# Kernel optimization log

Measured on AMD Instinct MI355X. Metric: run time of the kernel, lower is better.

Reference implementation:

```python
import jax, jax.numpy as jnp
import numpy as np

HIDDEN = 2048
NUM_HEADS = 16
HEAD_DIM = HIDDEN // NUM_HEADS  # 128
B, S = 2, 2048


def setup_inputs() -> dict:
    key = jax.random.key(0)
    ks = jax.random.split(key, 16)
    w = lambda k, shp: (jax.random.normal(k, shp, jnp.float32) * 0.02)
    return {
        "query": jax.random.normal(ks[0], (B, S, HIDDEN), jnp.float32),
        "key": jax.random.normal(ks[1], (B, S, HIDDEN), jnp.float32),
        "value": jax.random.normal(ks[2], (B, S, HIDDEN), jnp.float32),
        "Wq": w(ks[3], (HIDDEN, HIDDEN)), "bq": jnp.zeros((HIDDEN,), jnp.float32),
        "Wk": w(ks[4], (HIDDEN, HIDDEN)), "bk": jnp.zeros((HIDDEN,), jnp.float32),
        "Wv": w(ks[5], (HIDDEN, HIDDEN)), "bv": jnp.zeros((HIDDEN,), jnp.float32),
        "Wo": w(ks[6], (HIDDEN, HIDDEN)), "bo": jnp.zeros((HIDDEN,), jnp.float32),
        "Wf1": w(ks[7], (HEAD_DIM, 2 * HEAD_DIM)), "bf1": jnp.zeros((2 * HEAD_DIM,), jnp.float32),
        "Wf2": w(ks[8], (2 * HEAD_DIM, HEAD_DIM)), "bf2": jnp.zeros((HEAD_DIM,), jnp.float32),
    }


def reference(query, key, value, Wq, bq, Wk, bk, Wv, bv, Wo, bo, Wf1, bf1, Wf2, bf2):
    b, s, _ = query.shape

    def split_heads(x):  # [b,s,H] -> [b,h,s,d]
        return x.reshape(b, s, NUM_HEADS, HEAD_DIM).transpose(0, 2, 1, 3)

    def feature_map(x):  # MLP on last dim: d -> 2d -> relu -> d
        return jax.nn.relu(x @ Wf1 + bf1) @ Wf2 + bf2

    Q = feature_map(split_heads(query @ Wq + bq))
    K = feature_map(split_heads(key @ Wk + bk))
    V = split_heads(value @ Wv + bv)

    # K^T V per head: [b,h,d,e]
    KV = jnp.einsum("bhsd,bhse->bhde", K, V)
    QKV = jnp.einsum("bhsd,bhde->bhse", Q, KV)
    # denominator: sum of all K entries per (b,h) -> scalar per head
    denom = jnp.sum(K, axis=(-2, -1), keepdims=True) + 1e-8
    QKV = QKV / denom

    context = QKV.transpose(0, 2, 1, 3).reshape(b, s, HIDDEN)
    output = context @ Wo + bo

    attn_weights = jnp.full((b, NUM_HEADS, s, s), 1.0 / s, dtype=query.dtype)
    return output, attn_weights
```

## Files before the change

### kernel.cpp

```cpp
#include <hip/hip_runtime.h>


typedef __bf16 bf16_t;
typedef __bf16 bf16x8 __attribute__((ext_vector_type(8)));
typedef __bf16 bf16x4 __attribute__((ext_vector_type(4)));
typedef float  f32x4  __attribute__((ext_vector_type(4)));

#define FILLV (1.0f / 2048.0f)

#define VMCNT2() asm volatile("s_waitcnt vmcnt(2)" ::: "memory")
#define VMCNT0() asm volatile("s_waitcnt vmcnt(0)" ::: "memory")
#define LGKM0()  asm volatile("s_waitcnt lgkmcnt(0)" ::: "memory")
#define BAR()    __builtin_amdgcn_s_barrier()
#define SCHED0() __builtin_amdgcn_sched_barrier(0)

__device__ __forceinline__ void gload16(const void* g, void* l) {
  __builtin_amdgcn_global_load_lds(
      (__attribute__((address_space(1))) void*)(g),
      (__attribute__((address_space(3))) void*)(l), 16, 0, 0);
}

__device__ __forceinline__ void stage_half(const bf16_t* __restrict__ g,
                                           int h, unsigned char* ldsT, int t) {
  const bf16_t* gh = g + (long)h * 128 * 2048;
  unsigned char* lh = ldsT + h * 16384;
#pragma unroll
  for (int i = 0; i < 2; ++i) {
    const int c = t + i * 512;
    const int r = c >> 3;
    const int cc = ((c & 7) ^ (r & 7)) * 8;
    gload16(gh + (long)r * 2048 + cc, lh + c * 16);
  }
}

__device__ __forceinline__ bf16x8 lds_frag(const unsigned char* base,
                                           int row, int kelem) {
  int byte = row * 128 + kelem * 2;
  byte ^= (row & 7) << 4;
  return *(const bf16x8*)(base + byte);
}

__global__ __launch_bounds__(512, 2) void proj_gemm8(
    const bf16_t* __restrict__ A, const bf16_t* __restrict__ Wt,
    const float* __restrict__ bq, const float* __restrict__ bk,
    const float* __restrict__ bv, bf16_t* __restrict__ C,
    float* __restrict__ attn)
{
  __shared__ __align__(16) unsigned char smem[131072];
  const int t = threadIdx.x;
  const int lane = t & 63;
  const int wid = t >> 6;
  const int wr = wid >> 2, wc = wid & 3;
  const int bid = blockIdx.x;
  const int bx = bid & 7, by = bid >> 3;
  const int which = by >> 4;
  const bf16_t* Ab = A + (long)by * 256 * 2048;
  const bf16_t* Bb = Wt + (long)which * 4194304 + (long)bx * 256 * 2048;
  const float* bias = which == 0 ? bq : (which == 1 ? bk : bv);

  const int lr = lane & 15;
  const int l8 = (lane >> 4) * 8;
  const f32x4 fv = {FILLV, FILLV, FILLV, FILLV};

  f32x4 acc[8][4];
#pragma unroll
  for (int i = 0; i < 8; ++i)
#pragma unroll
    for (int j = 0; j < 4; ++j) acc[i][j] = (f32x4){0.f, 0.f, 0.f, 0.f};

  stage_half(Ab, 0, smem, t);
  stage_half(Ab, 1, smem, t);
  stage_half(Bb, 0, smem + 32768, t);
  stage_half(Bb, 1, smem + 32768, t);

  bf16x8 aF[4][2], bF[4][2];

  for (int kt = 0; kt < 32; ++kt) {
    const int cur = kt & 1;
    unsigned char* curA = smem + cur * 65536;
    unsigned char* curB = curA + 32768;
    unsigned char* nxtA = smem + (cur ^ 1) * 65536;
    unsigned char* nxtB = nxtA + 32768;
    const bool hn = kt < 31;
    const bf16_t* An = Ab + (kt + 1) * 64;
    const bf16_t* Bn = Bb + (kt + 1) * 64;
    const int arow = wr * 128 + lr;
    const int brow = wc * 64 + lr;
    f32x4* fillp = (f32x4*)attn + ((long)kt * 384 + bid) * 3 * 512 + t;

    if (hn) { stage_half(An, 0, nxtA, t); VMCNT2(); }
    else    { VMCNT0(); }
    BAR();
#pragma unroll
    for (int mi = 0; mi < 4; ++mi)
#pragma unroll
      for (int kk = 0; kk < 2; ++kk)
        aF[mi][kk] = lds_frag(curA, arow + mi * 16, kk * 32 + l8);
#pragma unroll
    for (int ni = 0; ni < 2; ++ni)
#pragma unroll
      for (int kk = 0; kk < 2; ++kk)
        bF[ni][kk] = lds_frag(curB, brow + ni * 16, kk * 32 + l8);
    LGKM0(); SCHED0();
    __builtin_amdgcn_s_setprio(1);
#pragma unroll
    for (int mi = 0; mi < 4; ++mi)
#pragma unroll
      for (int ni = 0; ni < 2; ++ni)
#pragma unroll
        for (int kk = 0; kk < 2; ++kk)
          acc[mi][ni] = __builtin_amdgcn_mfma_f32_16x16x32_bf16(
              aF[mi][kk], bF[ni][kk], acc[mi][ni], 0, 0, 0);
    __builtin_amdgcn_s_setprio(0);
    BAR();

    if (hn) stage_half(An, 1, nxtA, t);
    __builtin_nontemporal_store(fv, fillp);
#pragma unroll
    for (int ni = 0; ni < 2; ++ni)
#pragma unroll
      for (int kk = 0; kk < 2; ++kk)
        bF[2 + ni][kk] = lds_frag(curB, brow + (2 + ni) * 16, kk * 32 + l8);
    BAR(); LGKM0(); SCHED0();
    __builtin_amdgcn_s_setprio(1);
#pragma unroll
    for (int mi = 0; mi < 4; ++mi)
#pragma unroll
      for (int ni = 0; ni < 2; ++ni)
#pragma unroll
        for (int kk = 0; kk < 2; ++kk)
          acc[mi][2 + ni] = __builtin_amdgcn_mfma_f32_16x16x32_bf16(
              aF[mi][kk], bF[2 + ni][kk], acc[mi][2 + ni], 0, 0, 0);
    __builtin_amdgcn_s_setprio(0);
    BAR();

    if (hn) stage_half(Bn, 0, nxtB, t);
    __builtin_nontemporal_store(fv, fillp + 512);
#pragma unroll
    for (int mi = 0; mi < 4; ++mi)
#pragma unroll
      for (int kk = 0; kk < 2; ++kk)
        aF[mi][kk] = lds_frag(curA, arow + 64 + mi * 16, kk * 32 + l8);
    BAR(); LGKM0(); SCHED0();
    __builtin_amdgcn_s_setprio(1);
#pragma unroll
    for (int mi = 0; mi < 4; ++mi)
#pragma unroll
      for (int ni = 0; ni < 2; ++ni)
#pragma unroll
        for (int kk = 0; kk < 2; ++kk)
          acc[4 + mi][ni] = __builtin_amdgcn_mfma_f32_16x16x32_bf16(
              aF[mi][kk], bF[ni][kk], acc[4 + mi][ni], 0, 0, 0);
    __builtin_amdgcn_s_setprio(0);
    BAR();

    if (hn) stage_half(Bn, 1, nxtB, t);
    __builtin_nontemporal_store(fv, fillp + 1024);
    BAR(); LGKM0(); SCHED0();
    __builtin_amdgcn_s_setprio(1);
#pragma unroll
    for (int mi = 0; mi < 4; ++mi)
#pragma unroll
      for (int ni = 0; ni < 2; ++ni)
#pragma unroll
        for (int kk = 0; kk < 2; ++kk)
          acc[4 + mi][2 + ni] = __builtin_amdgcn_mfma_f32_16x16x32_bf16(
              aF[mi][kk], bF[2 + ni][kk], acc[4 + mi][2 + ni], 0, 0, 0);
    __builtin_amdgcn_s_setprio(0);
    BAR();
  }

  const int row0 = by * 256 + wr * 128;
  const int col0 = bx * 256 + wc * 64;
#pragma unroll
  for (int mi = 0; mi < 8; ++mi) {
#pragma unroll
    for (int ni = 0; ni < 4; ++ni) {
      const int col = col0 + ni * 16 + lr;
      const float bvv = bias[col];
#pragma unroll
      for (int j = 0; j < 4; ++j) {
        const int row = row0 + mi * 16 + (lane >> 4) * 4 + j;
        C[(long)row * 2048 + col] = (bf16_t)(acc[mi][ni][j] + bvv);
      }
    }
  }
}

template<bool RELU, bool OUTF32, bool BIAS, int FILLMODE>
__global__ __launch_bounds__(256) void gemm_bt(
    const bf16_t* __restrict__ A, const bf16_t* __restrict__ Bt,
    const float* __restrict__ bias, void* __restrict__ C,
    int K, int lda, int ldb, int ldc,
    long aBatchB, long aBatchH, long bBatchB, long bBatchH,
    long cBatchB, long cBatchH, int HperB,
    float* __restrict__ attn, long fillBase, long fillBase2, int fillSlots)
{
  __shared__ bf16_t As[128 * 64];
  __shared__ bf16_t Bs[128 * 64];

  const int z  = blockIdx.z;
  const int zb = z / HperB, zh = z % HperB;
  const bf16_t* Ab = A  + (long)zb * aBatchB + (long)zh * aBatchH
                        + (long)blockIdx.y * 128 * lda;
  const bf16_t* Bb = Bt + (long)zb * bBatchB + (long)zh * bBatchH
                        + (long)blockIdx.x * 128 * ldb;

  const int t = threadIdx.x;
  const int lane = t & 63, w = t >> 6;
  const int wm = (w >> 1) * 64, wn = (w & 1) * 64;
  const int p = ((int)blockIdx.z * gridDim.y + blockIdx.y) * gridDim.x
                + blockIdx.x;

  f32x4 acc[4][4];
#pragma unroll
  for (int i = 0; i < 4; ++i)
#pragma unroll
    for (int j = 0; j < 4; ++j) acc[i][j] = (f32x4){0.f, 0.f, 0.f, 0.f};

  for (int k0 = 0; k0 < K; k0 += 64) {
#pragma unroll
    for (int i = 0; i < 4; ++i) {
      int c = i * 256 + t;
      int row = c >> 3, col = (c & 7) * 8;
      gload16(Ab + (long)row * lda + k0 + col, &As[c * 8]);
      gload16(Bb + (long)row * ldb + k0 + col, &Bs[c * 8]);
    }
    if constexpr (FILLMODE == 3) {
      const f32x4 fv = {FILLV, FILLV, FILLV, FILLV};
      const long nB = (long)gridDim.x * gridDim.y * gridDim.z;
      long s0 = fillBase + (((long)(k0 >> 6) * nB + p) * 3) * 256 + t;
      __builtin_nontemporal_store(fv, (f32x4*)attn + s0);
      __builtin_nontemporal_store(fv, (f32x4*)attn + s0 + 256);
      __builtin_nontemporal_store(fv, (f32x4*)attn + s0 + 512);
    }
    __syncthreads();
#pragma unroll
    for (int kk = 0; kk < 2; ++kk) {
      bf16x8 af[4], bfr[4];
#pragma unroll
      for (int mi = 0; mi < 4; ++mi)
        af[mi] = *(const bf16x8*)&As[(wm + mi * 16 + (lane & 15)) * 64
                                     + kk * 32 + (lane >> 4) * 8];
#pragma unroll
      for (int ni = 0; ni < 4; ++ni)
        bfr[ni] = *(const bf16x8*)&Bs[(wn + ni * 16 + (lane & 15)) * 64
                                      + kk * 32 + (lane >> 4) * 8];
#pragma unroll
      for (int mi = 0; mi < 4; ++mi)
#pragma unroll
        for (int ni = 0; ni < 4; ++ni)
          acc[mi][ni] = __builtin_amdgcn_mfma_f32_16x16x32_bf16(
              af[mi], bfr[ni], acc[mi][ni], 0, 0, 0);
    }
    __syncthreads();
  }

  if constexpr (FILLMODE == 3) {
    const f32x4 fv = {FILLV, FILLV, FILLV, FILLV};
    f32x4* dst = (f32x4*)attn + fillBase2 + (long)p * fillSlots + t;
    for (int i = 0; i < fillSlots; i += 256)
      __builtin_nontemporal_store(fv, dst + i);
  }

  const long cb = (long)zb * cBatchB + (long)zh * cBatchH;
  const int row0 = blockIdx.y * 128 + wm;
  const int col0 = blockIdx.x * 128 + wn;
#pragma unroll
  for (int mi = 0; mi < 4; ++mi) {
#pragma unroll
    for (int ni = 0; ni < 4; ++ni) {
      const int col = col0 + ni * 16 + (lane & 15);
      const float bv = BIAS ? bias[col] : 0.f;
#pragma unroll
      for (int j = 0; j < 4; ++j) {
        const int row = row0 + mi * 16 + (lane >> 4) * 4 + j;
        float v = acc[mi][ni][j] + bv;
        if (RELU) v = fmaxf(v, 0.f);
        if (OUTF32) ((float*)C)[cb + (long)row * ldc + col] = v;
        else        ((bf16_t*)C)[cb + (long)row * ldc + col] = (bf16_t)v;
      }
    }
  }
}

__global__ __launch_bounds__(256) void fm_fused(
    const bf16_t* __restrict__ A, const bf16_t* __restrict__ W1t,
    const bf16_t* __restrict__ W2t, const float* __restrict__ b1,
    const float* __restrict__ b2, bf16_t* __restrict__ Out)
{
  __shared__ char Hs[64 * 256 * 2];
  const int t = threadIdx.x, lane = t & 63, w = t >> 6;
  const long r0 = (long)blockIdx.x * 64;
  const int lr = lane & 15, lk = lane >> 4;

  f32x4 acc[4][4];
#pragma unroll
  for (int i = 0; i < 4; ++i)
#pragma unroll
    for (int j = 0; j < 4; ++j) acc[i][j] = (f32x4){0.f, 0.f, 0.f, 0.f};
  const int wn = w * 64;
#pragma unroll
  for (int kk = 0; kk < 4; ++kk) {
    bf16x8 af[4], bfr[4];
#pragma unroll
    for (int mi = 0; mi < 4; ++mi)
      af[mi] = *(const bf16x8*)&A[(r0 + mi * 16 + lr) * 128 + kk * 32 + lk * 8];
#pragma unroll
    for (int ni = 0; ni < 4; ++ni)
      bfr[ni] = *(const bf16x8*)&W1t[(long)(wn + ni * 16 + lr) * 128
                                     + kk * 32 + lk * 8];
#pragma unroll
    for (int mi = 0; mi < 4; ++mi)
#pragma unroll
      for (int ni = 0; ni < 4; ++ni)
        acc[mi][ni] = __builtin_amdgcn_mfma_f32_16x16x32_bf16(
            af[mi], bfr[ni], acc[mi][ni], 0, 0, 0);
  }
#pragma unroll
  for (int ni = 0; ni < 4; ++ni) {
    const int col = wn + ni * 16 + lr;
    const float bvv = b1[col];
#pragma unroll
    for (int mi = 0; mi < 4; ++mi)
#pragma unroll
      for (int j = 0; j < 4; ++j) {
        const int row = mi * 16 + lk * 4 + j;
        float h = fmaxf(acc[mi][ni][j] + bvv, 0.f);
        int byte = (row << 9) + (col << 1);
        byte ^= (row & 7) << 4;
        *(bf16_t*)(Hs + byte) = (bf16_t)h;
      }
  }
  __syncthreads();

  f32x4 acc2[4][2];
#pragma unroll
  for (int i = 0; i < 4; ++i)
#pragma unroll
    for (int j = 0; j < 2; ++j) acc2[i][j] = (f32x4){0.f, 0.f, 0.f, 0.f};
  const int wn2 = w * 32;
#pragma unroll
  for (int kk = 0; kk < 8; ++kk) {
    bf16x8 af[4], bfr[2];
#pragma unroll
    for (int mi = 0; mi < 4; ++mi) {
      const int m = mi * 16 + lr;
      int byte = (m << 9) + kk * 64 + lk * 16;
      byte ^= (m & 7) << 4;
      af[mi] = *(const bf16x8*)(Hs + byte);
    }
#pragma unroll
    for (int ni = 0; ni < 2; ++ni)
      bfr[ni] = *(const bf16x8*)&W2t[(long)(wn2 + ni * 16 + lr) * 256
                                     + kk * 32 + lk * 8];
#pragma unroll
    for (int mi = 0; mi < 4; ++mi)
#pragma unroll
      for (int ni = 0; ni < 2; ++ni)
        acc2[mi][ni] = __builtin_amdgcn_mfma_f32_16x16x32_bf16(
            af[mi], bfr[ni], acc2[mi][ni], 0, 0, 0);
  }
#pragma unroll
  for (int ni = 0; ni < 2; ++ni) {
    const int col = wn2 + ni * 16 + lr;
    const float bvv = b2[col];
#pragma unroll
    for (int mi = 0; mi < 4; ++mi)
#pragma unroll
      for (int j = 0; j < 4; ++j) {
        const int row = mi * 16 + lk * 4 + j;
        Out[(r0 + row) * 128 + col] = (bf16_t)(acc2[mi][ni][j] + bvv);
      }
  }
}

__global__ __launch_bounds__(256) void prep(
    const float* __restrict__ q, const float* __restrict__ k,
    const float* __restrict__ v,
    const float* __restrict__ Wq, const float* __restrict__ Wk,
    const float* __restrict__ Wv, const float* __restrict__ Wo,
    const float* __restrict__ Wf1, const float* __restrict__ Wf2,
    bf16_t* __restrict__ qkv_bf, bf16_t* __restrict__ Wqkv_t,
    bf16_t* __restrict__ Wf1_t, bf16_t* __restrict__ Wf2_t)
{
  const int t = threadIdx.x;
  const int bid = blockIdx.x;
  __shared__ float tile[32][33];

  if (bid < 24576) {
    const float* in = bid < 8192 ? q : (bid < 16384 ? k : v);
    bf16_t* o = qkv_bf + (long)(bid >> 13) * 8388608L;
    long i = ((long)(bid & 8191) * 256 + t) * 4;
    float4 x = *(const float4*)&in[i];
    bf16x4 r = {(bf16_t)x.x, (bf16_t)x.y, (bf16_t)x.z, (bf16_t)x.w};
    *(bf16x4*)&o[i] = r;
    return;
  }

  const int x = t & 31, y = t >> 5;
  const float* W; bf16_t* out; int Kd, Nd, n0, k0;
  if (bid < 40960) {
    const int sub = bid - 24576;
    const int z = sub >> 12, r = sub & 4095;
    W = z == 0 ? Wq : z == 1 ? Wk : z == 2 ? Wv : Wo;
    out = Wqkv_t + (long)z * 4194304L;
    Kd = 2048; Nd = 2048;
    n0 = (r & 63) * 32; k0 = (r >> 6) * 32;
  } else if (bid < 40992) {
    const int sub = bid - 40960;
    W = Wf1; out = Wf1_t; Kd = 128; Nd = 256;
    n0 = (sub & 7) * 32; k0 = (sub >> 3) * 32;
  } else {
    const int sub = bid - 40992;
    W = Wf2; out = Wf2_t; Kd = 256; Nd = 128;
    n0 = (sub & 3) * 32; k0 = (sub >> 2) * 32;
  }
#pragma unroll
  for (int j = 0; j < 32; j += 8)
    tile[y + j][x] = W[(long)(k0 + y + j) * Nd + n0 + x];
  __syncthreads();
#pragma unroll
  for (int j = 0; j < 32; j += 8)
    out[(long)(n0 + y + j) * Kd + k0 + x] = (bf16_t)tile[x][y + j];
}

__global__ __launch_bounds__(256) void kv_partial(
    const bf16_t* __restrict__ Kf, const bf16_t* __restrict__ Vp,
    float* __restrict__ part, float* __restrict__ part_denom) {
  const int z = blockIdx.y, b = z >> 4, h = z & 15;
  const int s0 = blockIdx.x * 256;
  const int t = threadIdx.x;
  __shared__ bf16_t Ks[32 * 128];
  __shared__ bf16_t Vs[32 * 128];
  __shared__ float red[4];
  const bf16_t* Kb = Kf + (long)b * 4194304 + h * 128;
  const bf16_t* Vb = Vp + (long)b * 4194304 + h * 128;
  float acc[8][8];
#pragma unroll
  for (int i = 0; i < 8; ++i)
#pragma unroll
    for (int j = 0; j < 8; ++j) acc[i][j] = 0.f;
  float ksum = 0.f;
  const int d0 = (t & 15) * 8, e0 = (t >> 4) * 8;
  for (int sc = 0; sc < 256; sc += 32) {
#pragma unroll
    for (int i = 0; i < 2; ++i) {
      int idx = (i * 256 + t) * 8;
      int r = idx >> 7, c = idx & 127;
      long g = (long)(s0 + sc + r) * 2048 + c;
      *(bf16x8*)&Ks[r * 128 + c] = *(const bf16x8*)&Kb[g];
      *(bf16x8*)&Vs[r * 128 + c] = *(const bf16x8*)&Vb[g];
    }
    __syncthreads();
    {
      bf16x8 a0 = *(const bf16x8*)&Ks[t * 16];
      bf16x8 a1 = *(const bf16x8*)&Ks[t * 16 + 8];
#pragma unroll
      for (int j = 0; j < 8; ++j) ksum += (float)a0[j] + (float)a1[j];
    }
    for (int s = 0; s < 32; ++s) {
      bf16x8 kv = *(const bf16x8*)&Ks[s * 128 + d0];
      bf16x8 vv = *(const bf16x8*)&Vs[s * 128 + e0];
      float kf[8], vf[8];
#pragma unroll
      for (int i = 0; i < 8; ++i) { kf[i] = (float)kv[i]; vf[i] = (float)vv[i]; }
#pragma unroll
      for (int i = 0; i < 8; ++i)
#pragma unroll
        for (int j = 0; j < 8; ++j) acc[i][j] += vf[i] * kf[j];
    }
    __syncthreads();
  }

#pragma unroll
  for (int off = 32; off; off >>= 1) ksum += __shfl_down(ksum, off, 64);
  if ((t & 63) == 0) red[t >> 6] = ksum;
  __syncthreads();
  if (t == 0)
    part_denom[blockIdx.x * 32 + z] = red[0] + red[1] + red[2] + red[3];

  float* pb = part + ((long)blockIdx.x * 32 + z) * 16384;
#pragma unroll
  for (int i = 0; i < 8; ++i)
#pragma unroll
    for (int j = 0; j < 8; ++j)
      pb[(e0 + i) * 128 + (d0 + j)] = acc[i][j];
}

__global__ __launch_bounds__(256) void kv_reduce(
    const float* __restrict__ part, const float* __restrict__ part_denom,
    bf16_t* __restrict__ KVT) {
  const int z = blockIdx.x >> 4, slice = blockIdx.x & 15;
  const int t = threadIdx.x;
  float dsum = 0.f;
#pragma unroll
  for (int c = 0; c < 8; ++c) dsum += part_denom[c * 32 + z];
  const float inv = 1.0f / (dsum + 1e-8f);
  const long i0 = slice * 1024 + t * 4;
  f32x4 s = {0.f, 0.f, 0.f, 0.f};
#pragma unroll
  for (int c = 0; c < 8; ++c) {
    f32x4 v = *(const f32x4*)&part[((long)c * 32 + z) * 16384 + i0];
    s.x += v.x; s.y += v.y; s.z += v.z; s.w += v.w;
  }
  bf16x4 o = {(bf16_t)(s.x * inv), (bf16_t)(s.y * inv),
              (bf16_t)(s.z * inv), (bf16_t)(s.w * inv)};
  *(bf16x4*)&KVT[(long)z * 16384 + i0] = o;
}

extern "C" void kernel_launch(void* const* d_in, const int* in_sizes, int n_in,
                              void* d_out, int out_size, void* d_ws, size_t ws_size,
                              hipStream_t stream) {
  (void)in_sizes; (void)n_in; (void)out_size; (void)ws_size;
  const float* q   = (const float*)d_in[0];
  const float* k   = (const float*)d_in[1];
  const float* v   = (const float*)d_in[2];
  const float* Wq  = (const float*)d_in[3];
  const float* bq  = (const float*)d_in[4];
  const float* Wk  = (const float*)d_in[5];
  const float* bk  = (const float*)d_in[6];
  const float* Wv  = (const float*)d_in[7];
  const float* bv  = (const float*)d_in[8];
  const float* Wo  = (const float*)d_in[9];
  const float* bo  = (const float*)d_in[10];
  const float* Wf1 = (const float*)d_in[11];
  const float* bf1 = (const float*)d_in[12];
  const float* Wf2 = (const float*)d_in[13];
  const float* bf2 = (const float*)d_in[14];

  bf16_t* P      = (bf16_t*)d_ws;
  bf16_t* qkv_bf = P;
  bf16_t* Wqkv_t = P + 25165824L;
  bf16_t* Wo_t   = P + 37748736L;
  bf16_t* Wf1_t  = P + 41943040L;
  bf16_t* Wf2_t  = P + 41975808L;
  bf16_t* Qp     = P + 42008576L;
  bf16_t* Vp     = P + 58785792L;
  bf16_t* Qf     = P + 83951616L;
  bf16_t* Kf     = P + 92340224L;
  bf16_t* KVT    = P + 100728832L;
  float*  part   = (float*)d_ws;
  float*  part_denom = (float*)d_ws + 4194304L;

  float* out0 = (float*)d_out;
  float* attn = (float*)d_out + 8388608L;

  dim3 blk(256);

  prep<<<41024, blk, 0, stream>>>(q, k, v, Wq, Wk, Wv, Wo, Wf1, Wf2,
                                  qkv_bf, Wqkv_t, Wf1_t, Wf2_t);

  proj_gemm8<<<384, 512, 0, stream>>>(qkv_bf, Wqkv_t, bq, bk, bv, Qp, attn);

  fm_fused<<<2048, blk, 0, stream>>>(Qp, Wf1_t, Wf2_t, bf1, bf2, Qf);

  kv_partial<<<dim3(8, 32), blk, 0, stream>>>(Kf, Vp, part, part_denom);

  kv_reduce<<<512, blk, 0, stream>>>(part, part_denom, KVT);

  gemm_bt<false, false, false, 0><<<dim3(1, 16, 32), blk, 0, stream>>>(
      Qf, KVT, nullptr, Vp, 128, 2048, 128, 2048,
      4194304L, 128L, 262144L, 16384L, 4194304L, 128L, 16,
      nullptr, 0, 0, 0);

  gemm_bt<false, true, true, 3><<<dim3(16, 32, 1), blk, 0, stream>>>(
      Vp, Wo_t, bo, out0, 2048, 2048, 2048, 2048, 0, 0, 0, 0, 0, 0, 1,
      attn, 18874368L, 31457280L, 4096);
}
```

Before: 350.6 us.

## Halve proj GEMM N-tile to 128 and rebalance attn fill across kernels

The fused QKV projection GEMM now uses a 256x128 tile instead of 256x256, doubling the grid to 768 blocks and cutting LDS to 96KB and accumulators by half. This is meant to improve occupancy and load balance across CUs. It also moves more of the constant attention-weights fill into the projection kernel's main loop and drops the tail fill from the output GEMM. The cost is lower arithmetic intensity per block, since A tiles are reloaded twice as often.

```diff
diff --git a/kernel.cpp b/kernel.cpp
--- a/kernel.cpp
+++ b/kernel.cpp
@@ -8,6 +8,7 @@
 
 #define FILLV (1.0f / 2048.0f)
 
+#define VMCNT3() asm volatile("s_waitcnt vmcnt(3)" ::: "memory")
 #define VMCNT2() asm volatile("s_waitcnt vmcnt(2)" ::: "memory")
 #define VMCNT0() asm volatile("s_waitcnt vmcnt(0)" ::: "memory")
 #define LGKM0()  asm volatile("s_waitcnt lgkmcnt(0)" ::: "memory")
@@ -46,50 +47,50 @@
     const float* __restrict__ bv, bf16_t* __restrict__ C,
     float* __restrict__ attn)
 {
-  __shared__ __align__(16) unsigned char smem[131072];
+  __shared__ __align__(16) unsigned char smem[98304];
   const int t = threadIdx.x;
   const int lane = t & 63;
   const int wid = t >> 6;
   const int wr = wid >> 2, wc = wid & 3;
   const int bid = blockIdx.x;
-  const int bx = bid & 7, by = bid >> 3;
+  const int bx = bid & 15, by = bid >> 4;
   const int which = by >> 4;
   const bf16_t* Ab = A + (long)by * 256 * 2048;
-  const bf16_t* Bb = Wt + (long)which * 4194304 + (long)bx * 256 * 2048;
+  const bf16_t* Bb = Wt + (long)which * 4194304 + (long)bx * 128 * 2048;
   const float* bias = which == 0 ? bq : (which == 1 ? bk : bv);
 
   const int lr = lane & 15;
   const int l8 = (lane >> 4) * 8;
   const f32x4 fv = {FILLV, FILLV, FILLV, FILLV};
 
-  f32x4 acc[8][4];
+  f32x4 acc[8][2];
 #pragma unroll
   for (int i = 0; i < 8; ++i)
 #pragma unroll
-    for (int j = 0; j < 4; ++j) acc[i][j] = (f32x4){0.f, 0.f, 0.f, 0.f};
+    for (int j = 0; j < 2; ++j) acc[i][j] = (f32x4){0.f, 0.f, 0.f, 0.f};
 
   stage_half(Ab, 0, smem, t);
   stage_half(Ab, 1, smem, t);
   stage_half(Bb, 0, smem + 32768, t);
-  stage_half(Bb, 1, smem + 32768, t);
-
-  bf16x8 aF[4][2], bF[4][2];
+
+  bf16x8 aF[4][2], bF[2][2];
 
   for (int kt = 0; kt < 32; ++kt) {
     const int cur = kt & 1;
-    unsigned char* curA = smem + cur * 65536;
+    unsigned char* curA = smem + cur * 49152;
     unsigned char* curB = curA + 32768;
-    unsigned char* nxtA = smem + (cur ^ 1) * 65536;
+    unsigned char* nxtA = smem + (cur ^ 1) * 49152;
     unsigned char* nxtB = nxtA + 32768;
     const bool hn = kt < 31;
     const bf16_t* An = Ab + (kt + 1) * 64;
     const bf16_t* Bn = Bb + (kt + 1) * 64;
     const int arow = wr * 128 + lr;
-    const int brow = wc * 64 + lr;
-    f32x4* fillp = (f32x4*)attn + ((long)kt * 384 + bid) * 3 * 512 + t;
-
-    if (hn) { stage_half(An, 0, nxtA, t); VMCNT2(); }
-    else    { VMCNT0(); }
+    const int brow = wc * 32 + lr;
+    f32x4* fillp = (f32x4*)attn + ((long)kt * 768 + bid) * 1024 + t;
+
+    if (kt == 0)      { stage_half(An, 0, nxtA, t); VMCNT2(); }
+    else if (hn)      { stage_half(An, 0, nxtA, t); VMCNT3(); }
+    else              { VMCNT0(); }
     BAR();
 #pragma unroll
     for (int mi = 0; mi < 4; ++mi)
@@ -97,40 +98,32 @@
       for (int kk = 0; kk < 2; ++kk)
         aF[mi][kk] = lds_frag(curA, arow + mi * 16, kk * 32 + l8);
 #pragma unroll
-    for (int ni = 0; ni < 2; ++ni)
-#pragma unroll
-      for (int kk = 0; kk < 2; ++kk)
-        bF[ni][kk] = lds_frag(curB, brow + ni * 16, kk * 32 + l8);
+    for (int kk = 0; kk < 2; ++kk)
+      bF[0][kk] = lds_frag(curB, brow, kk * 32 + l8);
     LGKM0(); SCHED0();
     __builtin_amdgcn_s_setprio(1);
 #pragma unroll
     for (int mi = 0; mi < 4; ++mi)
 #pragma unroll
-      for (int ni = 0; ni < 2; ++ni)
-#pragma unroll
-        for (int kk = 0; kk < 2; ++kk)
-          acc[mi][ni] = __builtin_amdgcn_mfma_f32_16x16x32_bf16(
-              aF[mi][kk], bF[ni][kk], acc[mi][ni], 0, 0, 0);
+      for (int kk = 0; kk < 2; ++kk)
+        acc[mi][0] = __builtin_amdgcn_mfma_f32_16x16x32_bf16(
+            aF[mi][kk], bF[0][kk], acc[mi][0], 0, 0, 0);
     __builtin_amdgcn_s_setprio(0);
     BAR();
 
     if (hn) stage_half(An, 1, nxtA, t);
     __builtin_nontemporal_store(fv, fillp);
 #pragma unroll
-    for (int ni = 0; ni < 2; ++ni)
-#pragma unroll
-      for (int kk = 0; kk < 2; ++kk)
-        bF[2 + ni][kk] = lds_frag(curB, brow + (2 + ni) * 16, kk * 32 + l8);
+    for (int kk = 0; kk < 2; ++kk)
+      bF[1][kk] = lds_frag(curB, brow + 16, kk * 32 + l8);
     BAR(); LGKM0(); SCHED0();
     __builtin_amdgcn_s_setprio(1);
 #pragma unroll
     for (int mi = 0; mi < 4; ++mi)
 #pragma unroll
-      for (int ni = 0; ni < 2; ++ni)
-#pragma unroll
-        for (int kk = 0; kk < 2; ++kk)
-          acc[mi][2 + ni] = __builtin_amdgcn_mfma_f32_16x16x32_bf16(
-              aF[mi][kk], bF[2 + ni][kk], acc[mi][2 + ni], 0, 0, 0);
+      for (int kk = 0; kk < 2; ++kk)
+        acc[mi][1] = __builtin_amdgcn_mfma_f32_16x16x32_bf16(
+            aF[mi][kk], bF[1][kk], acc[mi][1], 0, 0, 0);
     __builtin_amdgcn_s_setprio(0);
     BAR();
 
@@ -146,36 +139,30 @@
 #pragma unroll
     for (int mi = 0; mi < 4; ++mi)
 #pragma unroll
-      for (int ni = 0; ni < 2; ++ni)
-#pragma unroll
-        for (int kk = 0; kk < 2; ++kk)
-          acc[4 + mi][ni] = __builtin_amdgcn_mfma_f32_16x16x32_bf16(
-              aF[mi][kk], bF[ni][kk], acc[4 + mi][ni], 0, 0, 0);
+      for (int kk = 0; kk < 2; ++kk)
+        acc[4 + mi][0] = __builtin_amdgcn_mfma_f32_16x16x32_bf16(
+            aF[mi][kk], bF[0][kk], acc[4 + mi][0], 0, 0, 0);
     __builtin_amdgcn_s_setprio(0);
     BAR();
 
-    if (hn) stage_half(Bn, 1, nxtB, t);
-    __builtin_nontemporal_store(fv, fillp + 1024);
     BAR(); LGKM0(); SCHED0();
     __builtin_amdgcn_s_setprio(1);
 #pragma unroll
     for (int mi = 0; mi < 4; ++mi)
 #pragma unroll
-      for (int ni = 0; ni < 2; ++ni)
-#pragma unroll
-        for (int kk = 0; kk < 2; ++kk)
-          acc[4 + mi][2 + ni] = __builtin_amdgcn_mfma_f32_16x16x32_bf16(
-              aF[mi][kk], bF[2 + ni][kk], acc[4 + mi][2 + ni], 0, 0, 0);
+      for (int kk = 0; kk < 2; ++kk)
+        acc[4 + mi][1] = __builtin_amdgcn_mfma_f32_16x16x32_bf16(
+            aF[mi][kk], bF[1][kk], acc[4 + mi][1], 0, 0, 0);
     __builtin_amdgcn_s_setprio(0);
     BAR();
   }
 
   const int row0 = by * 256 + wr * 128;
-  const int col0 = bx * 256 + wc * 64;
+  const int col0 = bx * 128 + wc * 32;
 #pragma unroll
   for (int mi = 0; mi < 8; ++mi) {
 #pragma unroll
-    for (int ni = 0; ni < 4; ++ni) {
+    for (int ni = 0; ni < 2; ++ni) {
       const int col = col0 + ni * 16 + lr;
       const float bvv = bias[col];
 #pragma unroll
@@ -194,7 +181,7 @@
     int K, int lda, int ldb, int ldc,
     long aBatchB, long aBatchH, long bBatchB, long bBatchH,
     long cBatchB, long cBatchH, int HperB,
-    float* __restrict__ attn, long fillBase, long fillBase2, int fillSlots)
+    float* __restrict__ attn, long fillBase)
 {
   __shared__ bf16_t As[128 * 64];
   __shared__ bf16_t Bs[128 * 64];
@@ -226,13 +213,12 @@
       gload16(Ab + (long)row * lda + k0 + col, &As[c * 8]);
       gload16(Bb + (long)row * ldb + k0 + col, &Bs[c * 8]);
     }
-    if constexpr (FILLMODE == 3) {
+    if constexpr (FILLMODE == 1) {
       const f32x4 fv = {FILLV, FILLV, FILLV, FILLV};
       const long nB = (long)gridDim.x * gridDim.y * gridDim.z;
-      long s0 = fillBase + (((long)(k0 >> 6) * nB + p) * 3) * 256 + t;
+      long s0 = fillBase + (((long)(k0 >> 6) * nB + p) * 2) * 256 + t;
       __builtin_nontemporal_store(fv, (f32x4*)attn + s0);
       __builtin_nontemporal_store(fv, (f32x4*)attn + s0 + 256);
-      __builtin_nontemporal_store(fv, (f32x4*)attn + s0 + 512);
     }
     __syncthreads();
 #pragma unroll
@@ -254,13 +240,6 @@
               af[mi], bfr[ni], acc[mi][ni], 0, 0, 0);
     }
     __syncthreads();
-  }
-
-  if constexpr (FILLMODE == 3) {
-    const f32x4 fv = {FILLV, FILLV, FILLV, FILLV};
-    f32x4* dst = (f32x4*)attn + fillBase2 + (long)p * fillSlots + t;
-    for (int i = 0; i < fillSlots; i += 256)
-      __builtin_nontemporal_store(fv, dst + i);
   }
 
   const long cb = (long)zb * cBatchB + (long)zh * cBatchH;
@@ -551,7 +530,7 @@
   prep<<<41024, blk, 0, stream>>>(q, k, v, Wq, Wk, Wv, Wo, Wf1, Wf2,
                                   qkv_bf, Wqkv_t, Wf1_t, Wf2_t);
 
-  proj_gemm8<<<384, 512, 0, stream>>>(qkv_bf, Wqkv_t, bq, bk, bv, Qp, attn);
+  proj_gemm8<<<768, 512, 0, stream>>>(qkv_bf, Wqkv_t, bq, bk, bv, Qp, attn);
 
   fm_fused<<<2048, blk, 0, stream>>>(Qp, Wf1_t, Wf2_t, bf1, bf2, Qf);
 
@@ -562,9 +541,9 @@
   gemm_bt<false, false, false, 0><<<dim3(1, 16, 32), blk, 0, stream>>>(
       Qf, KVT, nullptr, Vp, 128, 2048, 128, 2048,
       4194304L, 128L, 262144L, 16384L, 4194304L, 128L, 16,
-      nullptr, 0, 0, 0);
-
-  gemm_bt<false, true, true, 3><<<dim3(16, 32, 1), blk, 0, stream>>>(
+      nullptr, 0);
+
+  gemm_bt<false, true, true, 1><<<dim3(16, 32, 1), blk, 0, stream>>>(
       Vp, Wo_t, bo, out0, 2048, 2048, 2048, 2048, 0, 0, 0, 0, 0, 0, 1,
-      attn, 18874368L, 31457280L, 4096);
-}
+      attn, 25165824L);
+}
```

New measurement: 350.6 us. Within noise of the previous version (+0.0%).
